# Performance work log

Measured on AMD Instinct MI355X. Metric: run time of the kernel, lower is better.

## Reference

```python
import jax, jax.numpy as jnp
import numpy as np

D_PROJ = 256      # core d_proj
WIN = 1536        # win_small (mid path, L<=mid_thr)
STRIDE = 384      # stride_small


def setup_inputs() -> dict:
    key = jax.random.key(0)
    ks = jax.random.split(key, 6)
    B, L, d_h, T, d_g = 4, 8192, 1024, 512, 256
    H = jax.random.normal(ks[0], (B, L, d_h), jnp.float32)
    G = jax.random.normal(ks[1], (B, T, d_g), jnp.float32)
    attn_mask = jnp.ones((B, L), dtype=bool)
    Wq_core = jax.random.normal(ks[2], (d_g, D_PROJ), jnp.float32) / np.float32(np.sqrt(d_g))
    Wk_core = jax.random.normal(ks[3], (d_h, D_PROJ), jnp.float32) / np.float32(np.sqrt(d_h))
    Wq_win = jax.random.normal(ks[4], (d_g, d_h), jnp.float32) / np.float32(np.sqrt(d_g))
    Wk_win = jax.random.normal(ks[5], (d_h, d_h), jnp.float32) / np.float32(np.sqrt(d_h))
    return dict(H=H, G=G, attn_mask=attn_mask, Wq_core=Wq_core, Wk_core=Wk_core,
                Wq_win=Wq_win, Wk_win=Wk_win)


def _core_pool(Hk, G, mask, Wq_core, Wk_core):
    # GoSpecificWattiPooling: GO-query cross-attention pooling over residues.
    q = jnp.einsum('btg,gp->btp', G, Wq_core)                 # [B,T,P]
    k = jnp.einsum('bwd,dp->bwp', Hk, Wk_core)                # [B,W,P]
    scores = jnp.einsum('btp,bwp->btw', q, k) * (D_PROJ ** -0.5)
    scores = jnp.where(mask[:, None, :], scores, jnp.float32(-1e30))
    alpha = jax.nn.softmax(scores, axis=-1)                   # over residues
    return jnp.einsum('btw,bwd->btd', alpha, Hk)              # [B,T,d_h]


def _window_starts(L, win, stride):
    starts, s = [], 0
    while s < L:
        e = min(s + win, L)
        starts.append(s)
        if e == L:
            break
        s += stride
    return starts


def reference(H, G, attn_mask, Wq_core, Wk_core, Wq_win, Wk_win):
    B, L, D = H.shape
    T = G.shape[1]
    starts = jnp.asarray(_window_starts(L, WIN, STRIDE), jnp.int32)
    q_t = jnp.einsum('btg,gd->btd', G, Wq_win)                # [B,T,D]
    scale = D ** -0.5

    def step(carry, s0):
        m, ssum, z = carry
        Hk = jax.lax.dynamic_slice_in_dim(H, s0, WIN, axis=1)
        mk = jax.lax.dynamic_slice_in_dim(attn_mask, s0, WIN, axis=1)
        Zk = _core_pool(Hk, G, mk, Wq_core, Wk_core)          # [B,T,D]
        k_w = jnp.einsum('btd,de->bte', Zk, Wk_win)
        lw = (jnp.sum(q_t * k_w, axis=-1, keepdims=True) * scale).astype(jnp.float32)
        m_new = jnp.maximum(m, lw)
        exp_m = jnp.exp(m - m_new)
        exp_w = jnp.exp(lw - m_new)
        ssum = ssum * exp_m + exp_w
        z = z * exp_m + exp_w * Zk.astype(jnp.float32)
        return (m_new, ssum, z), None

    init = (jnp.full((B, T, 1), -jnp.inf, jnp.float32),
            jnp.zeros((B, T, 1), jnp.float32),
            jnp.zeros((B, T, D), jnp.float32))
    (m, ssum, z), _ = jax.lax.scan(step, init, starts)
    return (z / (ssum + 1e-8)).astype(H.dtype)
```

## Files before the change

### kernel.cpp

```cpp
#include <hip/hip_runtime.h>
#include <math.h>

constexpr int Bb = 4;
constexpr int Lb = 8192;
constexpr int Dh = 1024;
constexpr int Tt = 512;
constexpr int Dg = 256;
constexpr int Pp = 256;
constexpr int NW = 19;

typedef unsigned short u16;
typedef __bf16 bf16x8 __attribute__((ext_vector_type(8)));
typedef float f32x4 __attribute__((ext_vector_type(4)));
typedef unsigned short us8 __attribute__((ext_vector_type(8)));

__device__ __forceinline__ u16 f2bf(float x) {
  union { float f; unsigned u; } v;
  v.f = x;
  unsigned r = v.u + 0x7FFFu + ((v.u >> 16) & 1u);
  return (u16)(r >> 16);
}
__device__ __forceinline__ float bf2f(unsigned v) {
  union { unsigned u; float f; } c;
  c.u = v << 16;
  return c.f;
}

#define GLDS16(g, l)                                                          \
  __builtin_amdgcn_global_load_lds(                                           \
      (const __attribute__((address_space(1))) void*)(g),                     \
      (__attribute__((address_space(3))) void*)(l), 16, 0, 0)

__device__ __forceinline__ void stage_A(const u16* __restrict__ A, int lda,
                                        int bm, int kA, u16* As, int tid,
                                        int wid) {
  const int rr = tid >> 3;
  const int c16 = (tid & 7) ^ (rr & 7);
#pragma unroll
  for (int cc = 0; cc < 4; cc++) {
    const int r = cc * 64 + rr;
    GLDS16(A + (long long)(bm + r) * lda + kA + c16 * 8,
           As + cc * 4096 + wid * 512);
  }
}

__device__ __forceinline__ void stage_ops(const u16* __restrict__ A, int lda,
                                          int bm, int kA, u16* As,
                                          const u16* __restrict__ B, int ldb,
                                          int bn, int kB, u16* Bs, int tid,
                                          int wid) {
  stage_A(A, lda, bm, kA, As, tid, wid);
  stage_A(B, ldb, bn, kB, Bs, tid, wid);
}

template <int OB>
__global__ __launch_bounds__(512, 1) void gemm256(const u16* __restrict__ A,
                                                  const u16* __restrict__ B,
                                                  void* __restrict__ C,
                                                  int K, int lda, int ldb,
                                                  int ldc, long long sA,
                                                  long long sB, long long sC,
                                                  long long sK, int kSplit,
                                                  float alpha) {
  __shared__ u16 lds[65536];

  const int gx = gridDim.x, gy = gridDim.y;
  int flat = blockIdx.x + gx * (blockIdx.y + gy * blockIdx.z);
  const int nwg = gx * gy * (int)gridDim.z;
  const int q = nwg >> 3, r = nwg & 7;
  const int xcd = flat & 7, sub = flat >> 3;
  flat = (xcd < r ? xcd * (q + 1) : r * (q + 1) + (xcd - r) * q) + sub;
  const int bmI = flat % gx;
  const int t1 = flat / gx;
  const int bnI = t1 % gy;
  const int z = t1 / gy;

  const int b = z / kSplit, ks = z % kSplit;
  const int kLen = K / kSplit;
  const int nt = kLen >> 6;
  A += b * sA + (long long)ks * kLen;
  B += b * sB + (long long)ks * kLen;
  const long long cOff = (long long)b * sC + (long long)ks * sK;

  const int bm = bmI * 256, bn = bnI * 256;
  const int tid = threadIdx.x;
  const int wid = tid >> 6, l = tid & 63;
  const int wm = wid >> 2, wn = wid & 3;
  const int rl = l & 15, kq = l >> 4;
  const int xr = rl & 7;

  f32x4 acc[8][4];
#pragma unroll
  for (int i = 0; i < 8; i++)
#pragma unroll
    for (int j = 0; j < 4; j++) acc[i][j] = (f32x4){0.f, 0.f, 0.f, 0.f};

  stage_ops(A, lda, bm, 0, lds, B, ldb, bn, 0, lds + 32768, tid, wid);
  stage_ops(A, lda, bm, 64, lds + 16384, B, ldb, bn, 64, lds + 49152, tid, wid);
  asm volatile("s_waitcnt vmcnt(8)" ::: "memory");
  __builtin_amdgcn_s_barrier();

  for (int t = 0; t < nt; t++) {
    const int cur = t & 1;
    const u16* As = lds + cur * 16384;
    const u16* Bs = lds + 32768 + cur * 16384;
    bf16x8 a0[4][2], bb[4][2];

#pragma unroll
    for (int i = 0; i < 4; i++)
#pragma unroll
      for (int s = 0; s < 2; s++)
        a0[i][s] = *(const bf16x8*)(As + (wm * 128 + i * 16 + rl) * 64 +
                                    (((s * 4 + kq) ^ xr) << 3));
#pragma unroll
    for (int j = 0; j < 2; j++)
#pragma unroll
      for (int s = 0; s < 2; s++)
        bb[j][s] = *(const bf16x8*)(Bs + (wn * 64 + j * 16 + rl) * 64 +
                                    (((s * 4 + kq) ^ xr) << 3));
    __builtin_amdgcn_s_barrier();
    __builtin_amdgcn_s_setprio(1);
#pragma unroll
    for (int i = 0; i < 4; i++)
#pragma unroll
      for (int j = 0; j < 2; j++)
#pragma unroll
        for (int s = 0; s < 2; s++)
          acc[i][j] = __builtin_amdgcn_mfma_f32_16x16x32_bf16(
              a0[i][s], bb[j][s], acc[i][j], 0, 0, 0);
    __builtin_amdgcn_s_setprio(0);
    __builtin_amdgcn_s_barrier();

#pragma unroll
    for (int j = 2; j < 4; j++)
#pragma unroll
      for (int s = 0; s < 2; s++)
        bb[j][s] = *(const bf16x8*)(Bs + (wn * 64 + j * 16 + rl) * 64 +
                                    (((s * 4 + kq) ^ xr) << 3));
    __builtin_amdgcn_s_barrier();
    __builtin_amdgcn_s_setprio(1);
#pragma unroll
    for (int i = 0; i < 4; i++)
#pragma unroll
      for (int j = 2; j < 4; j++)
#pragma unroll
        for (int s = 0; s < 2; s++)
          acc[i][j] = __builtin_amdgcn_mfma_f32_16x16x32_bf16(
              a0[i][s], bb[j][s], acc[i][j], 0, 0, 0);
    __builtin_amdgcn_s_setprio(0);
    __builtin_amdgcn_s_barrier();

#pragma unroll
    for (int i = 0; i < 4; i++)
#pragma unroll
      for (int s = 0; s < 2; s++)
        a0[i][s] = *(const bf16x8*)(As + (wm * 128 + 64 + i * 16 + rl) * 64 +
                                    (((s * 4 + kq) ^ xr) << 3));
    __builtin_amdgcn_s_barrier();
    __builtin_amdgcn_s_setprio(1);
#pragma unroll
    for (int i = 0; i < 4; i++)
#pragma unroll
      for (int j = 2; j < 4; j++)
#pragma unroll
        for (int s = 0; s < 2; s++)
          acc[i + 4][j] = __builtin_amdgcn_mfma_f32_16x16x32_bf16(
              a0[i][s], bb[j][s], acc[i + 4][j], 0, 0, 0);
    __builtin_amdgcn_s_setprio(0);
    __builtin_amdgcn_s_barrier();

    if (t + 2 < nt) {
      u16* Asw = (u16*)lds + cur * 16384;
      u16* Bsw = (u16*)lds + 32768 + cur * 16384;
      stage_ops(A, lda, bm, (t + 2) * 64, Asw, B, ldb, bn, (t + 2) * 64, Bsw,
                tid, wid);
    }
    __builtin_amdgcn_s_setprio(1);
#pragma unroll
    for (int i = 0; i < 4; i++)
#pragma unroll
      for (int j = 0; j < 2; j++)
#pragma unroll
        for (int s = 0; s < 2; s++)
          acc[i + 4][j] = __builtin_amdgcn_mfma_f32_16x16x32_bf16(
              a0[i][s], bb[j][s], acc[i + 4][j], 0, 0, 0);
    __builtin_amdgcn_s_setprio(0);
    if (t + 2 < nt)
      asm volatile("s_waitcnt vmcnt(8)" ::: "memory");
    else
      asm volatile("s_waitcnt vmcnt(0)" ::: "memory");
    __builtin_amdgcn_s_barrier();
  }

  float* Cf = (float*)C;
  u16* Cb = (u16*)C;
#pragma unroll
  for (int i = 0; i < 8; i++) {
    const int row0 = bm + wm * 128 + i * 16 + kq * 4;
#pragma unroll
    for (int j = 0; j < 4; j++) {
      const int col = bn + wn * 64 + j * 16 + rl;
#pragma unroll
      for (int r2 = 0; r2 < 4; r2++) {
        const float v = alpha * acc[i][j][r2];
        const long long idx = cOff + (long long)(row0 + r2) * ldc + col;
        if (OB)
          Cb[idx] = f2bf(v);
        else
          Cf[idx] = v;
      }
    }
  }
}

__global__ __launch_bounds__(512, 1) void gemm256rb(const u16* __restrict__ A,
                                                    const u16* __restrict__ B,
                                                    float* __restrict__ C,
                                                    int K, int lda, int ldb,
                                                    int ldc, long long sA,
                                                    long long sB, long long sC,
                                                    long long sK, int kSplit,
                                                    float alpha) {
  __shared__ u16 lds[65536];

  const int gx = gridDim.x, gy = gridDim.y;
  int flat = blockIdx.x + gx * (blockIdx.y + gy * blockIdx.z);
  const int nwg = gx * gy * (int)gridDim.z;
  const int q = nwg >> 3, r = nwg & 7;
  const int xcd = flat & 7, sub = flat >> 3;
  flat = (xcd < r ? xcd * (q + 1) : r * (q + 1) + (xcd - r) * q) + sub;
  const int bmI = flat % gx;
  const int t1 = flat / gx;
  const int bnI = t1 % gy;
  const int z = t1 / gy;

  const int b = z / kSplit, ks = z % kSplit;
  const int kLen = K / kSplit;
  const int nt = kLen >> 6;
  A += b * sA + (long long)ks * kLen;
  B += b * sB + (long long)ks * kLen * (long long)ldb;
  const long long cOff = (long long)b * sC + (long long)ks * sK;

  const int bm = bmI * 256, bn = bnI * 256;
  const int tid = threadIdx.x;
  const int wid = tid >> 6, l = tid & 63;
  const int wm = wid >> 2, wn = wid & 3;
  const int rl = l & 15, kq = l >> 4;
  const int xr = rl & 7;

  const int bk = tid & 63;
  const int bj = (tid >> 6) * 4;
  const int bku = bk >> 3, bkl = bk & 7;

  f32x4 acc[8][4];
#pragma unroll
  for (int i = 0; i < 8; i++)
#pragma unroll
    for (int j = 0; j < 4; j++) acc[i][j] = (f32x4){0.f, 0.f, 0.f, 0.f};

  us8 br0[4], br1[4], breg[4];
#pragma unroll
  for (int c = 0; c < 4; c++)
    br0[c] = *(const us8*)(B + (long long)(0 * 64 + bk) * ldb + bn + (bj + c) * 8);
#pragma unroll
  for (int c = 0; c < 4; c++)
    br1[c] = *(const us8*)(B + (long long)(1 * 64 + bk) * ldb + bn + (bj + c) * 8);
  stage_A(A, lda, bm, 0, lds, tid, wid);
  stage_A(A, lda, bm, 64, lds + 16384, tid, wid);
  asm volatile("s_waitcnt vmcnt(8)" ::: "memory");
  {
    u16* B0 = (u16*)lds + 32768;
    u16* B1 = (u16*)lds + 49152;
#pragma unroll
    for (int c = 0; c < 4; c++)
#pragma unroll
      for (int i = 0; i < 8; i++) {
        const int nn = 8 * (bj + c) + i;
        const int off = nn * 64 + ((bku ^ i) << 3) + bkl;
        B0[off] = br0[c][i];
        B1[off] = br1[c][i];
      }
  }
  asm volatile("s_waitcnt vmcnt(0) lgkmcnt(0)" ::: "memory");
  __builtin_amdgcn_s_barrier();

  for (int t = 0; t < nt; t++) {
    const int cur = t & 1;
    const u16* As = lds + cur * 16384;
    const u16* Bs = lds + 32768 + cur * 16384;
    bf16x8 a0[4][2], bb[4][2];

    if (t + 2 < nt) {
#pragma unroll
      for (int c = 0; c < 4; c++)
        breg[c] = *(const us8*)(B + (long long)((t + 2) * 64 + bk) * ldb + bn +
                                (bj + c) * 8);
    }
#pragma unroll
    for (int i = 0; i < 4; i++)
#pragma unroll
      for (int s = 0; s < 2; s++)
        a0[i][s] = *(const bf16x8*)(As + (wm * 128 + i * 16 + rl) * 64 +
                                    (((s * 4 + kq) ^ xr) << 3));
#pragma unroll
    for (int j = 0; j < 2; j++)
#pragma unroll
      for (int s = 0; s < 2; s++)
        bb[j][s] = *(const bf16x8*)(Bs + (wn * 64 + j * 16 + rl) * 64 +
                                    (((s * 4 + kq) ^ xr) << 3));
    __builtin_amdgcn_s_barrier();
    __builtin_amdgcn_s_setprio(1);
#pragma unroll
    for (int i = 0; i < 4; i++)
#pragma unroll
      for (int j = 0; j < 2; j++)
#pragma unroll
        for (int s = 0; s < 2; s++)
          acc[i][j] = __builtin_amdgcn_mfma_f32_16x16x32_bf16(
              a0[i][s], bb[j][s], acc[i][j], 0, 0, 0);
    __builtin_amdgcn_s_setprio(0);
    __builtin_amdgcn_s_barrier();

#pragma unroll
    for (int j = 2; j < 4; j++)
#pragma unroll
      for (int s = 0; s < 2; s++)
        bb[j][s] = *(const bf16x8*)(Bs + (wn * 64 + j * 16 + rl) * 64 +
                                    (((s * 4 + kq) ^ xr) << 3));
    __builtin_amdgcn_s_barrier();
    __builtin_amdgcn_s_setprio(1);
#pragma unroll
    for (int i = 0; i < 4; i++)
#pragma unroll
      for (int j = 2; j < 4; j++)
#pragma unroll
        for (int s = 0; s < 2; s++)
          acc[i][j] = __builtin_amdgcn_mfma_f32_16x16x32_bf16(
              a0[i][s], bb[j][s], acc[i][j], 0, 0, 0);
    __builtin_amdgcn_s_setprio(0);
    __builtin_amdgcn_s_barrier();

#pragma unroll
    for (int i = 0; i < 4; i++)
#pragma unroll
      for (int s = 0; s < 2; s++)
        a0[i][s] = *(const bf16x8*)(As + (wm * 128 + 64 + i * 16 + rl) * 64 +
                                    (((s * 4 + kq) ^ xr) << 3));
    __builtin_amdgcn_s_barrier();
    __builtin_amdgcn_s_setprio(1);
#pragma unroll
    for (int i = 0; i < 4; i++)
#pragma unroll
      for (int j = 2; j < 4; j++)
#pragma unroll
        for (int s = 0; s < 2; s++)
          acc[i + 4][j] = __builtin_amdgcn_mfma_f32_16x16x32_bf16(
              a0[i][s], bb[j][s], acc[i + 4][j], 0, 0, 0);
    __builtin_amdgcn_s_setprio(0);
    __builtin_amdgcn_s_barrier();

    if (t + 2 < nt)
      stage_A(A, lda, bm, (t + 2) * 64, (u16*)lds + cur * 16384, tid, wid);
    __builtin_amdgcn_s_setprio(1);
#pragma unroll
    for (int i = 0; i < 4; i++)
#pragma unroll
      for (int j = 0; j < 2; j++)
#pragma unroll
        for (int s = 0; s < 2; s++)
          acc[i + 4][j] = __builtin_amdgcn_mfma_f32_16x16x32_bf16(
              a0[i][s], bb[j][s], acc[i + 4][j], 0, 0, 0);
    __builtin_amdgcn_s_setprio(0);
    if (t + 2 < nt) {
      asm volatile("s_waitcnt vmcnt(4)" ::: "memory");
      u16* Bw = (u16*)lds + 32768 + cur * 16384;
#pragma unroll
      for (int c = 0; c < 4; c++)
#pragma unroll
        for (int i = 0; i < 8; i++) {
          const int nn = 8 * (bj + c) + i;
          Bw[nn * 64 + ((bku ^ i) << 3) + bkl] = breg[c][i];
        }
      asm volatile("s_waitcnt lgkmcnt(0)" ::: "memory");
    } else {
      asm volatile("s_waitcnt vmcnt(0)" ::: "memory");
    }
    __builtin_amdgcn_s_barrier();
  }

#pragma unroll
  for (int i = 0; i < 8; i++) {
    const int row0 = bm + wm * 128 + i * 16 + kq * 4;
#pragma unroll
    for (int j = 0; j < 4; j++) {
      const int col = bn + wn * 64 + j * 16 + rl;
#pragma unroll
      for (int r2 = 0; r2 < 4; r2++) {
        const long long idx = cOff + (long long)(row0 + r2) * ldc + col;
        C[idx] = alpha * acc[i][j][r2];
      }
    }
  }
}

template <int OB, int ORD>
__global__ __launch_bounds__(256) void mgemm(const u16* __restrict__ A,
                                             const u16* __restrict__ B,
                                             void* __restrict__ C,
                                             int K, int lda, int ldb, int ldc,
                                             long long sA, long long sB,
                                             long long sC, long long sK,
                                             int kSplit, float alpha) {
  __shared__ u16 smem[8192];
  u16* As = smem;
  u16* Bs = smem + 4096;

  const int gx = gridDim.x, gy = gridDim.y;
  int flat = blockIdx.x + gx * (blockIdx.y + gy * blockIdx.z);
  const int nwg = gx * gy * (int)gridDim.z;
  const int q = nwg >> 3, r = nwg & 7;
  const int xcd = flat & 7, sub = flat >> 3;
  flat = (xcd < r ? xcd * (q + 1) : r * (q + 1) + (xcd - r) * q) + sub;
  int bmI, bnI, z;
  if (ORD == 0) {
    bmI = flat % gx;
    const int t = flat / gx;
    bnI = t % gy;
    z = t / gy;
  } else {
    bnI = flat % gy;
    const int t = flat / gy;
    bmI = t % gx;
    z = t / gx;
  }

  const int b = z / kSplit, ks = z % kSplit;
  const int kLen = K / kSplit;
  A += b * sA + (long long)ks * kLen;
  B += b * sB + (long long)ks * kLen;
  const long long cOff = (long long)b * sC + (long long)ks * sK;

  const int bm = bmI * 128;
  const int bn = bnI * 128;
  const int tid = threadIdx.x;
  const int l = tid & 63;
  const int wid = tid >> 6;
  const int wm = wid >> 1, wn = wid & 1;

  const int sr = l >> 2, sj = l & 3;
  const int skb = sj ^ ((sr >> 1) & 3);

  f32x4 acc[4][4];
#pragma unroll
  for (int i = 0; i < 4; i++)
#pragma unroll
    for (int j = 0; j < 4; j++) acc[i][j] = (f32x4){0.f, 0.f, 0.f, 0.f};

  const int rl = l & 15, kb = l >> 4;

  for (int k0 = 0; k0 < kLen; k0 += 32) {
    __syncthreads();
    {
      const int c1 = wid, c2 = wid + 4;
      GLDS16(A + (long long)(bm + c1 * 16 + sr) * lda + k0 + skb * 8,
             As + c1 * 512);
      GLDS16(A + (long long)(bm + c2 * 16 + sr) * lda + k0 + skb * 8,
             As + c2 * 512);
      GLDS16(B + (long long)(bn + c1 * 16 + sr) * ldb + k0 + skb * 8,
             Bs + c1 * 512);
      GLDS16(B + (long long)(bn + c2 * 16 + sr) * ldb + k0 + skb * 8,
             Bs + c2 * 512);
    }
    __syncthreads();

    bf16x8 af[4], bfr[4];
#pragma unroll
    for (int f = 0; f < 4; f++) {
      const int rowA = wm * 64 + f * 16 + rl;
      const int unitA = rowA * 4 + (kb ^ ((rowA >> 1) & 3));
      af[f] = *(const bf16x8*)(As + unitA * 8);
      const int rowB = wn * 64 + f * 16 + rl;
      const int unitB = rowB * 4 + (kb ^ ((rowB >> 1) & 3));
      bfr[f] = *(const bf16x8*)(Bs + unitB * 8);
    }
#pragma unroll
    for (int i = 0; i < 4; i++)
#pragma unroll
      for (int j = 0; j < 4; j++)
        acc[i][j] = __builtin_amdgcn_mfma_f32_16x16x32_bf16(af[i], bfr[j],
                                                            acc[i][j], 0, 0, 0);
  }

  float* Cf = (float*)C;
  u16* Cb = (u16*)C;
#pragma unroll
  for (int i = 0; i < 4; i++) {
    const int row0 = bm + wm * 64 + i * 16 + (l >> 4) * 4;
#pragma unroll
    for (int j = 0; j < 4; j++) {
      const int col = bn + wn * 64 + j * 16 + (l & 15);
#pragma unroll
      for (int r2 = 0; r2 < 4; r2++) {
        const float v = alpha * acc[i][j][r2];
        const long long idx = cOff + (long long)(row0 + r2) * ldc + col;
        if (OB)
          Cb[idx] = f2bf(v);
        else
          Cf[idx] = v;
      }
    }
  }
}

__global__ __launch_bounds__(256) void convk(const float* __restrict__ in,
                                             u16* __restrict__ out, long long n4) {
  for (long long i = (long long)blockIdx.x * 256 + threadIdx.x; i < n4;
       i += (long long)gridDim.x * 256) {
    const float4 v = ((const float4*)in)[i];
    ushort4 o;
    o.x = f2bf(v.x);
    o.y = f2bf(v.y);
    o.z = f2bf(v.z);
    o.w = f2bf(v.w);
    ((ushort4*)out)[i] = o;
  }
}

__global__ __launch_bounds__(256) void t32(const float* __restrict__ in,
                                           u16* __restrict__ out, int R, int C,
                                           long long sIn, long long sOut) {
  __shared__ float t[32][33];
  const int b = blockIdx.z;
  in += (long long)b * sIn;
  out += (long long)b * sOut;
  const int r0 = blockIdx.x * 32, c0 = blockIdx.y * 32;
  const int tx = threadIdx.x, ty = threadIdx.y;
#pragma unroll
  for (int i = 0; i < 4; i++)
    t[ty + i * 8][tx] = in[(long long)(r0 + ty + i * 8) * C + c0 + tx];
  __syncthreads();
#pragma unroll
  for (int i = 0; i < 4; i++)
    out[(long long)(c0 + ty + i * 8) * R + r0 + tx] = f2bf(t[tx][ty + i * 8]);
}

__global__ __launch_bounds__(256) void addout8(const float* __restrict__ p,
                                               float* __restrict__ out, long long n4) {
  for (long long i = (long long)blockIdx.x * 256 + threadIdx.x; i < n4;
       i += (long long)gridDim.x * 256) {
    float4 s = ((const float4*)p)[i];
#pragma unroll
    for (int j = 1; j < 8; j++) {
      const float4 v = ((const float4*)p)[i + (long long)j * n4];
      s.x += v.x;
      s.y += v.y;
      s.z += v.z;
      s.w += v.w;
    }
    ((float4*)out)[i] = s;
  }
}

__global__ __launch_bounds__(256) void combine2(const u16* __restrict__ SV,
                                                u16* __restrict__ Gm) {
  __shared__ u16 Ss[Lb];
  __shared__ float mx_s[64], se_s[64], sv_s[64], coef_s[64];
  __shared__ float m_s[NW], cw_s[NW];

  const int bt = blockIdx.x;
  const int b = bt >> 9, t = bt & 511;
  const u16* Srow = SV + ((long long)b * 1024 + t) * Lb;
  const u16* Vrow = SV + ((long long)b * 1024 + 512 + t) * Lb;
  u16* Grow = Gm + (long long)bt * Lb;

  const int tid = threadIdx.x;
  const int ln = tid & 63;
  const int wid = tid >> 6;

  for (int i = tid; i < Lb / 8; i += 256) {
    ((uint4*)Ss)[i] = ((const uint4*)Srow)[i];
  }
  __syncthreads();

  for (int i = 0; i < 16; i++) {
    const int c = wid * 16 + i;
    const int j0 = c * 128 + ln * 2;
    const unsigned sp = *(const unsigned*)&Ss[j0];
    const float s0 = bf2f(sp & 0xffffu), s1 = bf2f(sp >> 16);
    float mx = fmaxf(s0, s1);
#pragma unroll
    for (int o = 32; o; o >>= 1) mx = fmaxf(mx, __shfl_xor(mx, o, 64));
    const unsigned vv = *(const unsigned*)(Vrow + j0);
    const float v0 = bf2f(vv & 0xffffu), v1 = bf2f(vv >> 16);
    const float e0 = __expf(s0 - mx), e1 = __expf(s1 - mx);
    float se = e0 + e1;
    float sv = e0 * v0 + e1 * v1;
#pragma unroll
    for (int o = 32; o; o >>= 1) {
      se += __shfl_xor(se, o, 64);
      sv += __shfl_xor(sv, o, 64);
    }
    if (ln == 0) {
      mx_s[c] = mx;
      se_s[c] = se;
      sv_s[c] = sv;
    }
  }
  __syncthreads();

  if (wid == 0) {
    float lw = -1e30f, mw = 0.f, dw = 1.f;
    if (ln < NW) {
      const int c0 = (ln == 18) ? 52 : 3 * ln;
      mw = -1e30f;
#pragma unroll
      for (int k = 0; k < 12; k++) mw = fmaxf(mw, mx_s[c0 + k]);
      float d = 0.f, n = 0.f;
#pragma unroll
      for (int k = 0; k < 12; k++) {
        const float r = __expf(mx_s[c0 + k] - mw);
        d = fmaf(se_s[c0 + k], r, d);
        n = fmaf(sv_s[c0 + k], r, n);
      }
      dw = d;
      lw = (n / d) * 0.03125f;
    }
    float M = lw;
#pragma unroll
    for (int o = 32; o; o >>= 1) M = fmaxf(M, __shfl_xor(M, o, 64));
    const float e = (ln < NW) ? __expf(lw - M) : 0.f;
    float ss = e;
#pragma unroll
    for (int o = 32; o; o >>= 1) ss += __shfl_xor(ss, o, 64);
    if (ln < NW) {
      m_s[ln] = mw;
      cw_s[ln] = e / (ss + 1e-8f) / dw;
    }
  }
  __syncthreads();

  if (tid < 64) {
    const int c = tid;
    const int wlo = (c <= 11) ? 0 : (c - 9) / 3;
    const int whi = min(17, c / 3);
    const float mx = mx_s[c];
    float cf = 0.f;
    for (int w = wlo; w <= whi; w++) cf = fmaf(cw_s[w], __expf(mx - m_s[w]), cf);
    if (c >= 52) cf = fmaf(cw_s[18], __expf(mx - m_s[18]), cf);
    coef_s[c] = cf;
  }
  __syncthreads();

  for (int i = tid; i < Lb / 8; i += 256) {
    const int l0 = i * 8;
    const int c = l0 >> 7;
    const float mx = mx_s[c], cf = coef_s[c];
    const us8 sp = *(const us8*)&Ss[l0];
    us8 o;
#pragma unroll
    for (int j = 0; j < 8; j++)
      o[j] = f2bf(__expf(bf2f((unsigned)sp[j]) - mx) * cf);
    *(us8*)(Grow + l0) = o;
  }
}

extern "C" void kernel_launch(void* const* d_in, const int* in_sizes, int n_in,
                              void* d_out, int out_size, void* d_ws, size_t ws_size,
                              hipStream_t stream) {
  const float* H = (const float*)d_in[0];
  const float* G = (const float*)d_in[1];
  const float* Wq_core = (const float*)d_in[3];
  const float* Wk_core = (const float*)d_in[4];
  const float* Wq_win = (const float*)d_in[5];
  const float* Wk_win = (const float*)d_in[6];
  float* out = (float*)d_out;

  const size_t MB = (size_t)1 << 20;
  char* w = (char*)d_ws;
  u16* Hb    = (u16*)(w);
  u16* gb    = (u16*)(w + 64 * MB);
  u16* Asv   = (u16*)(w + 96 * MB);
  u16* SVb   = (u16*)(w + 128 * MB);
  float* part = (float*)(w + 128 * MB);
  u16* qb    = (u16*)(w + 192 * MB);
  u16* qtb   = (u16*)(w + 193 * MB);
  u16* Wkwb  = (u16*)(w + 197 * MB);
  u16* Wkcb  = (u16*)(w + 199 * MB);
  u16* WqcTb = (u16*)(w + 199 * MB + MB / 2);
  u16* WqwTb = (u16*)(w + 200 * MB);
  u16* Gb    = (u16*)(w + 201 * MB);

  convk<<<2048, 256, 0, stream>>>(H, Hb, (long long)Bb * Lb * Dh / 4);
  convk<<<256, 256, 0, stream>>>(Wk_core, Wkcb, (long long)Dh * Pp / 4);
  t32<<<dim3(8, 8, 1), dim3(32, 8), 0, stream>>>(Wq_core, WqcTb, Dg, Pp, 0, 0);
  t32<<<dim3(8, 32, 1), dim3(32, 8), 0, stream>>>(Wq_win, WqwTb, Dg, Dh, 0, 0);
  convk<<<1024, 256, 0, stream>>>(Wk_win, Wkwb, (long long)Dh * Dh / 4);
  convk<<<512, 256, 0, stream>>>(G, Gb, (long long)Bb * Tt * Dg / 4);

  mgemm<1, 0><<<dim3(16, 2, 1), 256, 0, stream>>>(
      Gb, WqcTb, qb, Dg, Dg, Dg, Pp, 0, 0, 0, 0, 1, 1.f);

  mgemm<1, 0><<<dim3(16, 8, 1), 256, 0, stream>>>(
      Gb, WqwTb, qtb, Dg, Dg, Dg, Dh, 0, 0, 0, 0, 1, 1.f);

  mgemm<1, 0><<<dim3(4, 8, Bb), 256, 0, stream>>>(
      qb, Wkcb, Asv, Pp, Pp, Pp, Dh, (long long)Tt * Pp, 0,
      (long long)1024 * Dh, 0, 1, 0.0625f);

  mgemm<1, 0><<<dim3(4, 8, Bb), 256, 0, stream>>>(
      qtb, Wkwb, Asv + (long long)512 * Dh, Dh, Dh, Dh, Dh,
      (long long)Tt * Dh, 0, (long long)1024 * Dh, 0, 1, 1.f);

  gemm256<1><<<dim3(4, 32, Bb), 512, 0, stream>>>(
      Asv, Hb, SVb, Dh, Dh, Dh, Lb, (long long)1024 * Dh,
      (long long)Lb * Dh, (long long)1024 * Lb, 0, 1, 1.f);

  combine2<<<dim3(Bb * Tt), 256, 0, stream>>>(SVb, gb);

  gemm256rb<<<dim3(2, 4, Bb * 8), 512, 0, stream>>>(
      gb, Hb, part, Lb, Lb, Dh, Dh, (long long)Tt * Lb, (long long)Lb * Dh,
      (long long)Tt * Dh, (long long)Bb * Tt * Dh, 8, 1.f);

  addout8<<<2048, 256, 0, stream>>>(part, out, (long long)Bb * Tt * Dh / 4);
}
```

Before: 270.2 us.

## Fuse H fp32-to-bf16 conversion into both large GEMMs' B-operand loads

Drops the standalone convk pass that turned all of H (128 MB fp32) into bf16. The two big GEMMs now read fp32 H directly into registers, convert to bf16 and write it swizzled into LDS, so the separate write and reread of a 64 MB bf16 copy goes away. In exchange each GEMM fetches twice as many bytes of H from global memory, and the new B path uses register-staged loads with a VALU conversion instead of direct global-to-LDS loads. That adds register pressure and can expose more load latency in the main loop.

Result: slower. 306.3 us (+13.3%).

```diff
diff --git a/kernel.cpp b/kernel.cpp
--- a/kernel.cpp
+++ b/kernel.cpp
@@ -25,6 +25,12 @@
   c.u = v << 16;
   return c.f;
 }
+__device__ __forceinline__ us8 cvt8(const float4 a, const float4 b) {
+  us8 o;
+  o[0] = f2bf(a.x); o[1] = f2bf(a.y); o[2] = f2bf(a.z); o[3] = f2bf(a.w);
+  o[4] = f2bf(b.x); o[5] = f2bf(b.y); o[6] = f2bf(b.z); o[7] = f2bf(b.w);
+  return o;
+}
 
 #define GLDS16(g, l)                                                          \
   __builtin_amdgcn_global_load_lds(                                           \
@@ -44,24 +50,208 @@
   }
 }
 
-__device__ __forceinline__ void stage_ops(const u16* __restrict__ A, int lda,
-                                          int bm, int kA, u16* As,
-                                          const u16* __restrict__ B, int ldb,
-                                          int bn, int kB, u16* Bs, int tid,
-                                          int wid) {
-  stage_A(A, lda, bm, kA, As, tid, wid);
-  stage_A(B, ldb, bn, kB, Bs, tid, wid);
-}
-
-template <int OB>
-__global__ __launch_bounds__(512, 1) void gemm256(const u16* __restrict__ A,
-                                                  const u16* __restrict__ B,
-                                                  void* __restrict__ C,
-                                                  int K, int lda, int ldb,
-                                                  int ldc, long long sA,
-                                                  long long sB, long long sC,
-                                                  long long sK, int kSplit,
-                                                  float alpha) {
+__global__ __launch_bounds__(512, 1) void gemm256cb(const u16* __restrict__ A,
+                                                    const float* __restrict__ Bf,
+                                                    u16* __restrict__ C,
+                                                    int K, int lda, int ldb,
+                                                    int ldc, long long sA,
+                                                    long long sB, long long sC,
+                                                    float alpha) {
+  __shared__ u16 lds[65536];
+
+  const int gx = gridDim.x, gy = gridDim.y;
+  int flat = blockIdx.x + gx * (blockIdx.y + gy * blockIdx.z);
+  const int nwg = gx * gy * (int)gridDim.z;
+  const int q = nwg >> 3, r = nwg & 7;
+  const int xcd = flat & 7, sub = flat >> 3;
+  flat = (xcd < r ? xcd * (q + 1) : r * (q + 1) + (xcd - r) * q) + sub;
+  const int bmI = flat % gx;
+  const int t1 = flat / gx;
+  const int bnI = t1 % gy;
+  const int b = t1 / gy;
+
+  const int nt = K >> 6;
+  A += (long long)b * sA;
+  Bf += (long long)b * sB;
+  const long long cOff = (long long)b * sC;
+
+  const int bm = bmI * 256, bn = bnI * 256;
+  const int tid = threadIdx.x;
+  const int wid = tid >> 6, l = tid & 63;
+  const int wm = wid >> 2, wn = wid & 3;
+  const int rl = l & 15, kq = l >> 4;
+  const int xr = rl & 7;
+
+  const int brow = tid >> 1;
+  const int bh = (tid & 1) * 4;
+  const int bkey = (brow & 7) << 3;
+
+  f32x4 acc[8][4];
+#pragma unroll
+  for (int i = 0; i < 8; i++)
+#pragma unroll
+    for (int j = 0; j < 4; j++) acc[i][j] = (f32x4){0.f, 0.f, 0.f, 0.f};
+
+  float4 b0f[8], b1f[8];
+#pragma unroll
+  for (int u2 = 0; u2 < 4; u2++) {
+    const float* s0 = Bf + (long long)(bn + brow) * ldb + (bh + u2) * 8;
+    b0f[u2 * 2] = *(const float4*)(s0);
+    b0f[u2 * 2 + 1] = *(const float4*)(s0 + 4);
+  }
+#pragma unroll
+  for (int u2 = 0; u2 < 4; u2++) {
+    const float* s1 = Bf + (long long)(bn + brow) * ldb + 64 + (bh + u2) * 8;
+    b1f[u2 * 2] = *(const float4*)(s1);
+    b1f[u2 * 2 + 1] = *(const float4*)(s1 + 4);
+  }
+  stage_A(A, lda, bm, 0, lds, tid, wid);
+  stage_A(A, lda, bm, 64, lds + 16384, tid, wid);
+  asm volatile("s_waitcnt vmcnt(8)" ::: "memory");
+  {
+    u16* B0 = (u16*)lds + 32768;
+    u16* B1 = (u16*)lds + 49152;
+#pragma unroll
+    for (int u2 = 0; u2 < 4; u2++) {
+      const int u = bh + u2;
+      const int off = brow * 64 + (((u ^ (brow & 7))) << 3);
+      *(us8*)(B0 + off) = cvt8(b0f[u2 * 2], b0f[u2 * 2 + 1]);
+      *(us8*)(B1 + off) = cvt8(b1f[u2 * 2], b1f[u2 * 2 + 1]);
+    }
+  }
+  asm volatile("s_waitcnt vmcnt(4) lgkmcnt(0)" ::: "memory");
+  __builtin_amdgcn_s_barrier();
+
+  for (int t = 0; t < nt; t++) {
+    const int cur = t & 1;
+    const u16* As = lds + cur * 16384;
+    const u16* Bs = lds + 32768 + cur * 16384;
+    bf16x8 a0[4][2], bb[4][2];
+    float4 bregf[8];
+
+    if (t + 2 < nt) {
+#pragma unroll
+      for (int u2 = 0; u2 < 4; u2++) {
+        const float* src =
+            Bf + (long long)(bn + brow) * ldb + (t + 2) * 64 + (bh + u2) * 8;
+        bregf[u2 * 2] = *(const float4*)(src);
+        bregf[u2 * 2 + 1] = *(const float4*)(src + 4);
+      }
+    }
+#pragma unroll
+    for (int i = 0; i < 4; i++)
+#pragma unroll
+      for (int s = 0; s < 2; s++)
+        a0[i][s] = *(const bf16x8*)(As + (wm * 128 + i * 16 + rl) * 64 +
+                                    (((s * 4 + kq) ^ xr) << 3));
+#pragma unroll
+    for (int j = 0; j < 2; j++)
+#pragma unroll
+      for (int s = 0; s < 2; s++)
+        bb[j][s] = *(const bf16x8*)(Bs + (wn * 64 + j * 16 + rl) * 64 +
+                                    (((s * 4 + kq) ^ xr) << 3));
+    __builtin_amdgcn_s_barrier();
+    __builtin_amdgcn_s_setprio(1);
+#pragma unroll
+    for (int i = 0; i < 4; i++)
+#pragma unroll
+      for (int j = 0; j < 2; j++)
+#pragma unroll
+        for (int s = 0; s < 2; s++)
+          acc[i][j] = __builtin_amdgcn_mfma_f32_16x16x32_bf16(
+              a0[i][s], bb[j][s], acc[i][j], 0, 0, 0);
+    __builtin_amdgcn_s_setprio(0);
+    __builtin_amdgcn_s_barrier();
+
+#pragma unroll
+    for (int j = 2; j < 4; j++)
+#pragma unroll
+      for (int s = 0; s < 2; s++)
+        bb[j][s] = *(const bf16x8*)(Bs + (wn * 64 + j * 16 + rl) * 64 +
+                                    (((s * 4 + kq) ^ xr) << 3));
+    __builtin_amdgcn_s_barrier();
+    __builtin_amdgcn_s_setprio(1);
+#pragma unroll
+    for (int i = 0; i < 4; i++)
+#pragma unroll
+      for (int j = 2; j < 4; j++)
+#pragma unroll
+        for (int s = 0; s < 2; s++)
+          acc[i][j] = __builtin_amdgcn_mfma_f32_16x16x32_bf16(
+              a0[i][s], bb[j][s], acc[i][j], 0, 0, 0);
+    __builtin_amdgcn_s_setprio(0);
+    __builtin_amdgcn_s_barrier();
+
+#pragma unroll
+    for (int i = 0; i < 4; i++)
+#pragma unroll
+      for (int s = 0; s < 2; s++)
+        a0[i][s] = *(const bf16x8*)(As + (wm * 128 + 64 + i * 16 + rl) * 64 +
+                                    (((s * 4 + kq) ^ xr) << 3));
+    __builtin_amdgcn_s_barrier();
+    __builtin_amdgcn_s_setprio(1);
+#pragma unroll
+    for (int i = 0; i < 4; i++)
+#pragma unroll
+      for (int j = 2; j < 4; j++)
+#pragma unroll
+        for (int s = 0; s < 2; s++)
+          acc[i + 4][j] = __builtin_amdgcn_mfma_f32_16x16x32_bf16(
+              a0[i][s], bb[j][s], acc[i + 4][j], 0, 0, 0);
+    __builtin_amdgcn_s_setprio(0);
+    __builtin_amdgcn_s_barrier();
+
+    if (t + 2 < nt)
+      stage_A(A, lda, bm, (t + 2) * 64, (u16*)lds + cur * 16384, tid, wid);
+    __builtin_amdgcn_s_setprio(1);
+#pragma unroll
+    for (int i = 0; i < 4; i++)
+#pragma unroll
+      for (int j = 0; j < 2; j++)
+#pragma unroll
+        for (int s = 0; s < 2; s++)
+          acc[i + 4][j] = __builtin_amdgcn_mfma_f32_16x16x32_bf16(
+              a0[i][s], bb[j][s], acc[i + 4][j], 0, 0, 0);
+    __builtin_amdgcn_s_setprio(0);
+    if (t + 2 < nt) {
+      asm volatile("s_waitcnt vmcnt(4)" ::: "memory");
+      u16* Bw = (u16*)lds + 32768 + cur * 16384;
+#pragma unroll
+      for (int u2 = 0; u2 < 4; u2++) {
+        const int u = bh + u2;
+        *(us8*)(Bw + brow * 64 + ((u ^ (brow & 7)) << 3)) =
+            cvt8(bregf[u2 * 2], bregf[u2 * 2 + 1]);
+      }
+      asm volatile("s_waitcnt lgkmcnt(0)" ::: "memory");
+    } else {
+      asm volatile("s_waitcnt vmcnt(0)" ::: "memory");
+    }
+    __builtin_amdgcn_s_barrier();
+  }
+
+#pragma unroll
+  for (int i = 0; i < 8; i++) {
+    const int row0 = bm + wm * 128 + i * 16 + kq * 4;
+#pragma unroll
+    for (int j = 0; j < 4; j++) {
+      const int col = bn + wn * 64 + j * 16 + rl;
+#pragma unroll
+      for (int r2 = 0; r2 < 4; r2++) {
+        const long long idx = cOff + (long long)(row0 + r2) * ldc + col;
+        C[idx] = f2bf(alpha * acc[i][j][r2]);
+      }
+    }
+  }
+}
+
+__global__ __launch_bounds__(512, 1) void gemm256rb(const u16* __restrict__ A,
+                                                    const float* __restrict__ Bf,
+                                                    float* __restrict__ C,
+                                                    int K, int lda, int ldb,
+                                                    int ldc, long long sA,
+                                                    long long sB, long long sC,
+                                                    long long sK, int kSplit,
+                                                    float alpha) {
   __shared__ u16 lds[65536];
 
   const int gx = gridDim.x, gy = gridDim.y;
@@ -79,7 +269,7 @@
   const int kLen = K / kSplit;
   const int nt = kLen >> 6;
   A += b * sA + (long long)ks * kLen;
-  B += b * sB + (long long)ks * kLen;
+  Bf += b * sB + (long long)ks * kLen * (long long)ldb;
   const long long cOff = (long long)b * sC + (long long)ks * sK;
 
   const int bm = bmI * 256, bn = bnI * 256;
@@ -89,165 +279,6 @@
   const int rl = l & 15, kq = l >> 4;
   const int xr = rl & 7;
 
-  f32x4 acc[8][4];
-#pragma unroll
-  for (int i = 0; i < 8; i++)
-#pragma unroll
-    for (int j = 0; j < 4; j++) acc[i][j] = (f32x4){0.f, 0.f, 0.f, 0.f};
-
-  stage_ops(A, lda, bm, 0, lds, B, ldb, bn, 0, lds + 32768, tid, wid);
-  stage_ops(A, lda, bm, 64, lds + 16384, B, ldb, bn, 64, lds + 49152, tid, wid);
-  asm volatile("s_waitcnt vmcnt(8)" ::: "memory");
-  __builtin_amdgcn_s_barrier();
-
-  for (int t = 0; t < nt; t++) {
-    const int cur = t & 1;
-    const u16* As = lds + cur * 16384;
-    const u16* Bs = lds + 32768 + cur * 16384;
-    bf16x8 a0[4][2], bb[4][2];
-
-#pragma unroll
-    for (int i = 0; i < 4; i++)
-#pragma unroll
-      for (int s = 0; s < 2; s++)
-        a0[i][s] = *(const bf16x8*)(As + (wm * 128 + i * 16 + rl) * 64 +
-                                    (((s * 4 + kq) ^ xr) << 3));
-#pragma unroll
-    for (int j = 0; j < 2; j++)
-#pragma unroll
-      for (int s = 0; s < 2; s++)
-        bb[j][s] = *(const bf16x8*)(Bs + (wn * 64 + j * 16 + rl) * 64 +
-                                    (((s * 4 + kq) ^ xr) << 3));
-    __builtin_amdgcn_s_barrier();
-    __builtin_amdgcn_s_setprio(1);
-#pragma unroll
-    for (int i = 0; i < 4; i++)
-#pragma unroll
-      for (int j = 0; j < 2; j++)
-#pragma unroll
-        for (int s = 0; s < 2; s++)
-          acc[i][j] = __builtin_amdgcn_mfma_f32_16x16x32_bf16(
-              a0[i][s], bb[j][s], acc[i][j], 0, 0, 0);
-    __builtin_amdgcn_s_setprio(0);
-    __builtin_amdgcn_s_barrier();
-
-#pragma unroll
-    for (int j = 2; j < 4; j++)
-#pragma unroll
-      for (int s = 0; s < 2; s++)
-        bb[j][s] = *(const bf16x8*)(Bs + (wn * 64 + j * 16 + rl) * 64 +
-                                    (((s * 4 + kq) ^ xr) << 3));
-    __builtin_amdgcn_s_barrier();
-    __builtin_amdgcn_s_setprio(1);
-#pragma unroll
-    for (int i = 0; i < 4; i++)
-#pragma unroll
-      for (int j = 2; j < 4; j++)
-#pragma unroll
-        for (int s = 0; s < 2; s++)
-          acc[i][j] = __builtin_amdgcn_mfma_f32_16x16x32_bf16(
-              a0[i][s], bb[j][s], acc[i][j], 0, 0, 0);
-    __builtin_amdgcn_s_setprio(0);
-    __builtin_amdgcn_s_barrier();
-
-#pragma unroll
-    for (int i = 0; i < 4; i++)
-#pragma unroll
-      for (int s = 0; s < 2; s++)
-        a0[i][s] = *(const bf16x8*)(As + (wm * 128 + 64 + i * 16 + rl) * 64 +
-                                    (((s * 4 + kq) ^ xr) << 3));
-    __builtin_amdgcn_s_barrier();
-    __builtin_amdgcn_s_setprio(1);
-#pragma unroll
-    for (int i = 0; i < 4; i++)
-#pragma unroll
-      for (int j = 2; j < 4; j++)
-#pragma unroll
-        for (int s = 0; s < 2; s++)
-          acc[i + 4][j] = __builtin_amdgcn_mfma_f32_16x16x32_bf16(
-              a0[i][s], bb[j][s], acc[i + 4][j], 0, 0, 0);
-    __builtin_amdgcn_s_setprio(0);
-    __builtin_amdgcn_s_barrier();
-
-    if (t + 2 < nt) {
-      u16* Asw = (u16*)lds + cur * 16384;
-      u16* Bsw = (u16*)lds + 32768 + cur * 16384;
-      stage_ops(A, lda, bm, (t + 2) * 64, Asw, B, ldb, bn, (t + 2) * 64, Bsw,
-                tid, wid);
-    }
-    __builtin_amdgcn_s_setprio(1);
-#pragma unroll
-    for (int i = 0; i < 4; i++)
-#pragma unroll
-      for (int j = 0; j < 2; j++)
-#pragma unroll
-        for (int s = 0; s < 2; s++)
-          acc[i + 4][j] = __builtin_amdgcn_mfma_f32_16x16x32_bf16(
-              a0[i][s], bb[j][s], acc[i + 4][j], 0, 0, 0);
-    __builtin_amdgcn_s_setprio(0);
-    if (t + 2 < nt)
-      asm volatile("s_waitcnt vmcnt(8)" ::: "memory");
-    else
-      asm volatile("s_waitcnt vmcnt(0)" ::: "memory");
-    __builtin_amdgcn_s_barrier();
-  }
-
-  float* Cf = (float*)C;
-  u16* Cb = (u16*)C;
-#pragma unroll
-  for (int i = 0; i < 8; i++) {
-    const int row0 = bm + wm * 128 + i * 16 + kq * 4;
-#pragma unroll
-    for (int j = 0; j < 4; j++) {
-      const int col = bn + wn * 64 + j * 16 + rl;
-#pragma unroll
-      for (int r2 = 0; r2 < 4; r2++) {
-        const float v = alpha * acc[i][j][r2];
-        const long long idx = cOff + (long long)(row0 + r2) * ldc + col;
-        if (OB)
-          Cb[idx] = f2bf(v);
-        else
-          Cf[idx] = v;
-      }
-    }
-  }
-}
-
-__global__ __launch_bounds__(512, 1) void gemm256rb(const u16* __restrict__ A,
-                                                    const u16* __restrict__ B,
-                                                    float* __restrict__ C,
-                                                    int K, int lda, int ldb,
-                                                    int ldc, long long sA,
-                                                    long long sB, long long sC,
-                                                    long long sK, int kSplit,
-                                                    float alpha) {
-  __shared__ u16 lds[65536];
-
-  const int gx = gridDim.x, gy = gridDim.y;
-  int flat = blockIdx.x + gx * (blockIdx.y + gy * blockIdx.z);
-  const int nwg = gx * gy * (int)gridDim.z;
-  const int q = nwg >> 3, r = nwg & 7;
-  const int xcd = flat & 7, sub = flat >> 3;
-  flat = (xcd < r ? xcd * (q + 1) : r * (q + 1) + (xcd - r) * q) + sub;
-  const int bmI = flat % gx;
-  const int t1 = flat / gx;
-  const int bnI = t1 % gy;
-  const int z = t1 / gy;
-
-  const int b = z / kSplit, ks = z % kSplit;
-  const int kLen = K / kSplit;
-  const int nt = kLen >> 6;
-  A += b * sA + (long long)ks * kLen;
-  B += b * sB + (long long)ks * kLen * (long long)ldb;
-  const long long cOff = (long long)b * sC + (long long)ks * sK;
-
-  const int bm = bmI * 256, bn = bnI * 256;
-  const int tid = threadIdx.x;
-  const int wid = tid >> 6, l = tid & 63;
-  const int wm = wid >> 2, wn = wid & 3;
-  const int rl = l & 15, kq = l >> 4;
-  const int xr = rl & 7;
-
   const int bk = tid & 63;
   const int bj = (tid >> 6) * 4;
   const int bku = bk >> 3, bkl = bk & 7;
@@ -258,13 +289,19 @@
 #pragma unroll
     for (int j = 0; j < 4; j++) acc[i][j] = (f32x4){0.f, 0.f, 0.f, 0.f};
 
-  us8 br0[4], br1[4], breg[4];
-#pragma unroll
-  for (int c = 0; c < 4; c++)
-    br0[c] = *(const us8*)(B + (long long)(0 * 64 + bk) * ldb + bn + (bj + c) * 8);
-#pragma unroll
-  for (int c = 0; c < 4; c++)
-    br1[c] = *(const us8*)(B + (long long)(1 * 64 + bk) * ldb + bn + (bj + c) * 8);
+  float4 br0f[8], br1f[8], bregf[8];
+#pragma unroll
+  for (int c = 0; c < 4; c++) {
+    const float* s0 = Bf + (long long)(0 * 64 + bk) * ldb + bn + (bj + c) * 8;
+    br0f[c * 2] = *(const float4*)(s0);
+    br0f[c * 2 + 1] = *(const float4*)(s0 + 4);
+  }
+#pragma unroll
+  for (int c = 0; c < 4; c++) {
+    const float* s1 = Bf + (long long)(1 * 64 + bk) * ldb + bn + (bj + c) * 8;
+    br1f[c * 2] = *(const float4*)(s1);
+    br1f[c * 2 + 1] = *(const float4*)(s1 + 4);
+  }
   stage_A(A, lda, bm, 0, lds, tid, wid);
   stage_A(A, lda, bm, 64, lds + 16384, tid, wid);
   asm volatile("s_waitcnt vmcnt(8)" ::: "memory");
@@ -272,14 +309,17 @@
     u16* B0 = (u16*)lds + 32768;
     u16* B1 = (u16*)lds + 49152;
 #pragma unroll
-    for (int c = 0; c < 4; c++)
+    for (int c = 0; c < 4; c++) {
+      const us8 o0 = cvt8(br0f[c * 2], br0f[c * 2 + 1]);
+      const us8 o1 = cvt8(br1f[c * 2], br1f[c * 2 + 1]);
 #pragma unroll
       for (int i = 0; i < 8; i++) {
         const int nn = 8 * (bj + c) + i;
         const int off = nn * 64 + ((bku ^ i) << 3) + bkl;
-        B0[off] = br0[c][i];
-        B1[off] = br1[c][i];
-      }
+        B0[off] = o0[i];
+        B1[off] = o1[i];
+      }
+    }
   }
   asm volatile("s_waitcnt vmcnt(0) lgkmcnt(0)" ::: "memory");
   __builtin_amdgcn_s_barrier();
@@ -292,9 +332,12 @@
 
     if (t + 2 < nt) {
 #pragma unroll
-      for (int c = 0; c < 4; c++)
-        breg[c] = *(const us8*)(B + (long long)((t + 2) * 64 + bk) * ldb + bn +
-                                (bj + c) * 8);
+      for (int c = 0; c < 4; c++) {
+        const float* src =
+            Bf + (long long)((t + 2) * 64 + bk) * ldb + bn + (bj + c) * 8;
+        bregf[c * 2] = *(const float4*)(src);
+        bregf[c * 2 + 1] = *(const float4*)(src + 4);
+      }
     }
 #pragma unroll
     for (int i = 0; i < 4; i++)
@@ -375,12 +418,14 @@
       asm volatile("s_waitcnt vmcnt(4)" ::: "memory");
       u16* Bw = (u16*)lds + 32768 + cur * 16384;
 #pragma unroll
-      for (int c = 0; c < 4; c++)
+      for (int c = 0; c < 4; c++) {
+        const us8 o = cvt8(bregf[c * 2], bregf[c * 2 + 1]);
 #pragma unroll
         for (int i = 0; i < 8; i++) {
           const int nn = 8 * (bj + c) + i;
-          Bw[nn * 64 + ((bku ^ i) << 3) + bkl] = breg[c][i];
+          Bw[nn * 64 + ((bku ^ i) << 3) + bkl] = o[i];
         }
+      }
       asm volatile("s_waitcnt lgkmcnt(0)" ::: "memory");
     } else {
       asm volatile("s_waitcnt vmcnt(0)" ::: "memory");
@@ -677,7 +722,6 @@
 
   const size_t MB = (size_t)1 << 20;
   char* w = (char*)d_ws;
-  u16* Hb    = (u16*)(w);
   u16* gb    = (u16*)(w + 64 * MB);
   u16* Asv   = (u16*)(w + 96 * MB);
   u16* SVb   = (u16*)(w + 128 * MB);
@@ -690,7 +734,6 @@
   u16* WqwTb = (u16*)(w + 200 * MB);
   u16* Gb    = (u16*)(w + 201 * MB);
 
-  convk<<<2048, 256, 0, stream>>>(H, Hb, (long long)Bb * Lb * Dh / 4);
   convk<<<256, 256, 0, stream>>>(Wk_core, Wkcb, (long long)Dh * Pp / 4);
   t32<<<dim3(8, 8, 1), dim3(32, 8), 0, stream>>>(Wq_core, WqcTb, Dg, Pp, 0, 0);
   t32<<<dim3(8, 32, 1), dim3(32, 8), 0, stream>>>(Wq_win, WqwTb, Dg, Dh, 0, 0);
@@ -711,14 +754,14 @@
       qtb, Wkwb, Asv + (long long)512 * Dh, Dh, Dh, Dh, Dh,
       (long long)Tt * Dh, 0, (long long)1024 * Dh, 0, 1, 1.f);
 
-  gemm256<1><<<dim3(4, 32, Bb), 512, 0, stream>>>(
-      Asv, Hb, SVb, Dh, Dh, Dh, Lb, (long long)1024 * Dh,
-      (long long)Lb * Dh, (long long)1024 * Lb, 0, 1, 1.f);
+  gemm256cb<<<dim3(4, 32, Bb), 512, 0, stream>>>(
+      Asv, H, SVb, Dh, Dh, Dh, Lb, (long long)1024 * Dh,
+      (long long)Lb * Dh, (long long)1024 * Lb, 1.f);
 
   combine2<<<dim3(Bb * Tt), 256, 0, stream>>>(SVb, gb);
 
   gemm256rb<<<dim3(2, 4, Bb * 8), 512, 0, stream>>>(
-      gb, Hb, part, Lb, Lb, Dh, Dh, (long long)Tt * Lb, (long long)Lb * Dh,
+      gb, H, part, Lb, Lb, Dh, Dh, (long long)Tt * Lb, (long long)Lb * Dh,
       (long long)Tt * Dh, (long long)Bb * Tt * Dh, 8, 1.f);
 
   addout8<<<2048, 256, 0, stream>>>(part, out, (long long)Bb * Tt * Dh / 4);
```
